# Kernel tuning notes

Measured on AMD Instinct MI355X. Metric: run time of the kernel, lower is better.

## Reference

```python
import jax, jax.numpy as jnp
import numpy as np

N = 30000
E = 960000
F_IN = 16
NH1 = 36
NH2 = 36
KH = 8
IN_POOL = 2
OUT_POOL = 2
NUM_CLASSES = 10
RATIO = 0.1
EPS = 1e-5


def cheb_conv(x, src, dst, valid, W, b):
    """PyG ChebConv with sym normalization, lambda_max=2 -> L_hat = -D^-1/2 A D^-1/2.
    W: [K, in, out], valid: float mask [E] for (soft-)deleted edges."""
    n = x.shape[0]
    deg = jax.ops.segment_sum(valid, src, num_segments=n)
    dinv = jnp.where(deg > 0, jax.lax.rsqrt(deg), 0.0)
    norm = dinv[src] * dinv[dst] * valid  # [E]

    def prop(h):  # L_hat @ h
        return -jax.ops.segment_sum(norm[:, None] * h[src], dst, num_segments=n)

    k_hops = W.shape[0]
    tx0 = x
    out = tx0 @ W[0]
    if k_hops > 1:
        tx1 = prop(tx0)
        out = out + tx1 @ W[1]
        for kk in range(2, k_hops):
            tx2 = 2.0 * prop(tx1) - tx0
            out = out + tx2 @ W[kk]
            tx0, tx1 = tx1, tx2
    return out + b


def batch_norm(x, gamma, beta):
    mu = jnp.mean(x, axis=0)
    var = jnp.var(x, axis=0)
    return (x - mu) * jax.lax.rsqrt(var + EPS) * gamma + beta


def setup_inputs() -> dict:
    key = jax.random.key(0)
    ks = jax.random.split(key, 20)
    rn = lambda k, s: jax.random.normal(k, s, dtype=jnp.float32) * 0.1
    x = jax.random.normal(ks[0], (N, F_IN), dtype=jnp.float32)
    edge_index = jax.random.randint(ks[1], (2, E), 0, N, dtype=jnp.int32)
    return {
        "x": x,
        "edge_index": edge_index,
        "W1": rn(ks[2], (KH, F_IN, NH1)), "b1": jnp.zeros((NH1,), jnp.float32),
        "W2": rn(ks[3], (KH, NH1, NH2)), "b2": jnp.zeros((NH2,), jnp.float32),
        "g1": jnp.ones((NH1,), jnp.float32), "be1": jnp.zeros((NH1,), jnp.float32),
        "g2": jnp.ones((NH2,), jnp.float32), "be2": jnp.zeros((NH2,), jnp.float32),
        "Wc": rn(ks[4], (1, NH1, IN_POOL)), "bc": jnp.zeros((IN_POOL,), jnp.float32),
        "pool_w": rn(ks[5], (IN_POOL,)),
        "Wp": rn(ks[6], (KH, IN_POOL, OUT_POOL)), "bp": jnp.zeros((OUT_POOL,), jnp.float32),
        "W3": rn(ks[7], (1, NH1 + NH2 + OUT_POOL, NUM_CLASSES)),
        "b3": jnp.zeros((NUM_CLASSES,), jnp.float32),
    }


def reference(x, edge_index, W1, b1, W2, b2, g1, be1, g2, be2, Wc, bc, pool_w, Wp, bp, W3, b3):
    src, dst = edge_index[0], edge_index[1]
    valid = jnp.ones((src.shape[0],), jnp.float32)

    x1 = batch_norm(jax.nn.relu(cheb_conv(x, src, dst, valid, W1, b1)), g1, be1)
    x2 = batch_norm(jax.nn.relu(cheb_conv(x1, src, dst, valid, W2, b2)), g2, be2)
    xc = cheb_conv(x1, src, dst, valid, Wc, bc)

    # TopKPooling(ratio=0.1)
    score = jnp.tanh(xc @ pool_w / jnp.linalg.norm(pool_w))  # [N]
    k = int(np.ceil(RATIO * x.shape[0]))
    _, perm = jax.lax.top_k(score, k)
    xp1 = xc[perm] * score[perm][:, None]
    new_idx = jnp.full((x.shape[0],), -1, jnp.int32).at[perm].set(jnp.arange(k, dtype=jnp.int32))
    vs, vd = new_idx[src], new_idx[dst]
    valid_p = ((vs >= 0) & (vd >= 0)).astype(jnp.float32)
    src_p = jnp.where(vs >= 0, vs, 0)
    dst_p = jnp.where(vd >= 0, vd, 0)

    xp2 = cheb_conv(xp1, src_p, dst_p, valid_p, Wp, bp)  # [k, OUT_POOL]

    # nearest-neighbor unpooling using last-2 feature columns as 2D positions
    pos = x[:, -2:]              # [N, 2]
    pos_p = pos[perm]            # [k, 2]
    d2 = jnp.sum((pos[:, None, :] - pos_p[None, :, :]) ** 2, axis=-1)  # [N, k]
    nearest = jnp.argmin(d2, axis=1)
    x3u = xp2[nearest]           # [N, OUT_POOL]

    h = jnp.concatenate((x1, x2, x3u), axis=1)
    return cheb_conv(h, src, dst, valid, W3, b3)
```

## Files before the change

kernel.cpp:

```cpp
#include <hip/hip_runtime.h>
#include <cstdint>

constexpr int NN   = 30000;
constexpr int NE   = 960000;
constexpr int FIN  = 16;
constexpr int H1   = 36;
constexpr int H2   = 36;
constexpr int KHOP = 8;
constexpr int KSEL = 3000;
constexpr int PCAP = 32768;
constexpr int NCHUNK = 12;
constexpr int CHUNK = KSEL / NCHUNK;
constexpr int NB_H = 32;
constexpr int EPB  = (NE + NB_H - 1) / NB_H;
constexpr float EPSV = 1e-5f;

#define TPB 256

static inline int nb(long long t) { return (int)((t + TPB - 1) / TPB); }

__global__ void k_dinv2(const int* __restrict__ cnt, float* __restrict__ dinv, int n) {
    int i = blockIdx.x * blockDim.x + threadIdx.x;
    if (i < n) { int v = cnt[i]; dinv[i] = v > 0 ? rsqrtf((float)v) : 0.0f; }
}

__global__ __launch_bounds__(1024)
void k_hist(const int* __restrict__ src, const int* __restrict__ dst,
            int* __restrict__ partials, int* __restrict__ rank) {
    __shared__ int hist[NN];
    for (int j = threadIdx.x; j < NN; j += 1024) hist[j] = 0;
    __syncthreads();
    int b = blockIdx.x;
    int e0 = b * EPB, e1 = min(NE, e0 + EPB);
    if (blockIdx.y == 0) {
        for (int e = e0 + (int)threadIdx.x; e < e1; e += 1024)
            atomicAdd(&hist[src[e]], 1);
    } else {
        for (int e = e0 + (int)threadIdx.x; e < e1; e += 1024)
            rank[e] = atomicAdd(&hist[dst[e]], 1);
    }
    __syncthreads();
    int* P = partials + ((size_t)blockIdx.y * NB_H + b) * NN;
    for (int j = threadIdx.x; j < NN; j += 1024) P[j] = hist[j];
}

__global__ void k_red(int* __restrict__ partials, float* __restrict__ dinv,
                      int* __restrict__ cnt_dst) {
    int j = blockIdx.x * blockDim.x + threadIdx.x;
    if (j >= NN) return;
    const int* Ps = partials;
    int s = 0;
#pragma unroll
    for (int b = 0; b < NB_H; ++b) s += Ps[(size_t)b * NN + j];
    dinv[j] = s > 0 ? rsqrtf((float)s) : 0.0f;
    int* Pd = partials + (size_t)NB_H * NN;
    int run = 0;
#pragma unroll
    for (int b = 0; b < NB_H; ++b) {
        int t = Pd[(size_t)b * NN + j];
        Pd[(size_t)b * NN + j] = run;
        run += t;
    }
    cnt_dst[j] = run;
}

__device__ __forceinline__ int block_scan_excl_1024(int val, int& total) {
    __shared__ int wsum[16];
    int tid = threadIdx.x, lane = tid & 63, wv = tid >> 6;
    int v = val;
#pragma unroll
    for (int off = 1; off < 64; off <<= 1) {
        int t = __shfl_up(v, off, 64);
        if (lane >= off) v += t;
    }
    __syncthreads();
    if (lane == 63) wsum[wv] = v;
    __syncthreads();
    if (tid < 16) {
        int w = wsum[tid];
#pragma unroll
        for (int off = 1; off < 16; off <<= 1) {
            int t = __shfl_up(w, off, 64);
            if (tid >= off) w += t;
        }
        wsum[tid] = w;
    }
    __syncthreads();
    int base = (wv > 0) ? wsum[wv - 1] : 0;
    total = wsum[15];
    return base + v - val;
}

__global__ void k_scan(const int* __restrict__ cnt, int* __restrict__ rowstart, int n) {
    __shared__ int run;
    if (threadIdx.x == 0) run = 0;
    __syncthreads();
    for (int base = 0; base < n; base += 1024) {
        int i = base + threadIdx.x;
        int v = (i < n) ? cnt[i] : 0;
        int tot; int ex = block_scan_excl_1024(v, tot);
        int r = run;
        if (i < n) rowstart[i] = r + ex;
        __syncthreads();
        if (threadIdx.x == 0) run += tot;
        __syncthreads();
    }
    if (threadIdx.x == 0) rowstart[n] = run;
}

__global__ void k_fill3(const int* __restrict__ src, const int* __restrict__ dst,
                        const int* __restrict__ rank, const float* __restrict__ dinv,
                        const int* __restrict__ rowstart, const int* __restrict__ Pd_excl,
                        int2* __restrict__ csr, int E) {
    int e = blockIdx.x * blockDim.x + threadIdx.x;
    if (e >= E) return;
    int s = src[e], d = dst[e];
    int b = e / EPB;
    int pos = rowstart[d] + Pd_excl[(size_t)b * NN + d] + rank[e];
    float w = -dinv[s] * dinv[d];
    csr[pos] = make_int2(s, __float_as_int(w));
}

template<int F, int O>
__global__ void k_gemm_init(const float* __restrict__ in, const float* __restrict__ W,
                            const float* __restrict__ b, float* __restrict__ acc, int n) {
    __shared__ float sW[F * O];
    for (int i = threadIdx.x; i < F * O; i += blockDim.x) sW[i] = W[i];
    __syncthreads();
    int t = blockIdx.x * blockDim.x + threadIdx.x;
    if (t >= n * O) return;
    int node = t / O, o = t - node * O;
    const float* r = &in[node * F];
    float s = b[o];
#pragma unroll
    for (int f = 0; f < F; ++f) s = fmaf(r[f], sW[f * O + o], s);
    acc[t] = s;
}

template<int F, int O, int BN>
__global__ __launch_bounds__(BN * F / 4)
void k_prop_gemm(const int* __restrict__ rowstart, const int2* __restrict__ csr,
                 const float* __restrict__ h, const float* __restrict__ t0,
                 const float* __restrict__ W, float* __restrict__ tout,
                 float* __restrict__ acc, int n, int first) {
    constexpr int QF = F / 4;
    constexpr int NT = BN * QF;
    __shared__ float sT[BN * F];
    __shared__ float sW[F * O];
    const int tid = threadIdx.x;
    for (int i = tid; i < F * O; i += NT) sW[i] = W[i];
    const int nl = tid / QF, q = tid - nl * QF;
    const int node = blockIdx.x * BN + nl;
    if (node < n) {
        const float4* __restrict__ h4 = (const float4*)h;
        float4 p = {0.f, 0.f, 0.f, 0.f};
        int e0 = rowstart[node], e1 = rowstart[node + 1];
        int e = e0;
        for (; e + 3 < e1; e += 4) {
            int2 ea = csr[e];
            int2 eb = csr[e + 1];
            int2 ec = csr[e + 2];
            int2 ed = csr[e + 3];
            float4 ha = h4[ea.x * QF + q];
            float4 hb = h4[eb.x * QF + q];
            float4 hc = h4[ec.x * QF + q];
            float4 hd = h4[ed.x * QF + q];
            float wa = __int_as_float(ea.y), wb = __int_as_float(eb.y);
            float wc = __int_as_float(ec.y), wd = __int_as_float(ed.y);
            p.x = fmaf(wa, ha.x, p.x); p.y = fmaf(wa, ha.y, p.y);
            p.z = fmaf(wa, ha.z, p.z); p.w = fmaf(wa, ha.w, p.w);
            p.x = fmaf(wb, hb.x, p.x); p.y = fmaf(wb, hb.y, p.y);
            p.z = fmaf(wb, hb.z, p.z); p.w = fmaf(wb, hb.w, p.w);
            p.x = fmaf(wc, hc.x, p.x); p.y = fmaf(wc, hc.y, p.y);
            p.z = fmaf(wc, hc.z, p.z); p.w = fmaf(wc, hc.w, p.w);
            p.x = fmaf(wd, hd.x, p.x); p.y = fmaf(wd, hd.y, p.y);
            p.z = fmaf(wd, hd.z, p.z); p.w = fmaf(wd, hd.w, p.w);
        }
        for (; e < e1; ++e) {
            int2 ew = csr[e];
            float w = __int_as_float(ew.y);
            float4 hv = h4[ew.x * QF + q];
            p.x = fmaf(w, hv.x, p.x); p.y = fmaf(w, hv.y, p.y);
            p.z = fmaf(w, hv.z, p.z); p.w = fmaf(w, hv.w, p.w);
        }
        if (!first) {
            float4 tv = ((const float4*)t0)[node * QF + q];
            p.x = 2.f * p.x - tv.x; p.y = 2.f * p.y - tv.y;
            p.z = 2.f * p.z - tv.z; p.w = 2.f * p.w - tv.w;
        }
        ((float4*)tout)[node * QF + q] = p;
        sT[nl * F + 4 * q + 0] = p.x; sT[nl * F + 4 * q + 1] = p.y;
        sT[nl * F + 4 * q + 2] = p.z; sT[nl * F + 4 * q + 3] = p.w;
    }
    __syncthreads();
    for (int idx = tid; idx < BN * O; idx += NT) {
        int nl2 = idx / O, o = idx - nl2 * O;
        int gn = blockIdx.x * BN + nl2;
        if (gn >= n) break;
        float s = 0.f;
#pragma unroll
        for (int f = 0; f < F; ++f) s = fmaf(sT[nl2 * F + f], sW[f * O + o], s);
        acc[gn * O + o] += s;
    }
}

template<int C>
__global__ void k_colstats(const float* __restrict__ a, float* __restrict__ stats, int n) {
    __shared__ float b1[C], b2[C];
    for (int i = threadIdx.x; i < C; i += blockDim.x) { b1[i] = 0.f; b2[i] = 0.f; }
    __syncthreads();
    int t0 = blockIdx.x * blockDim.x + threadIdx.x;
    int stride = gridDim.x * blockDim.x;
    int c = t0 % C;
    float s1 = 0.f, s2 = 0.f;
    for (int t = t0; t < n * C; t += stride) {
        float v = fmaxf(a[t], 0.f);
        s1 += v; s2 = fmaf(v, v, s2);
    }
    atomicAdd(&b1[c], s1); atomicAdd(&b2[c], s2);
    __syncthreads();
    for (int i = threadIdx.x; i < C; i += blockDim.x) {
        atomicAdd(&stats[i], b1[i]); atomicAdd(&stats[C + i], b2[i]);
    }
}

template<int C>
__global__ void k_bn(const float* __restrict__ a, const float* __restrict__ stats,
                     const float* __restrict__ g, const float* __restrict__ be,
                     float* __restrict__ o, int n) {
    int t = blockIdx.x * blockDim.x + threadIdx.x;
    if (t >= n * C) return;
    int c = t % C;
    float mu = stats[c] / n;
    float var = stats[C + c] / n - mu * mu;
    float v = fmaxf(a[t], 0.f);
    o[t] = (v - mu) * rsqrtf(var + EPSV) * g[c] + be[c];
}

__global__ void k_xc_score(const float* __restrict__ x1, const float* __restrict__ Wc,
                           const float* __restrict__ bc, const float* __restrict__ pw,
                           float* __restrict__ xc, float* __restrict__ score,
                           unsigned* __restrict__ key, int* __restrict__ gh, int n) {
    int i = blockIdx.x * blockDim.x + threadIdx.x;
    if (i >= n) return;
    const float* r = &x1[i * H1];
    float a = bc[0], b = bc[1];
#pragma unroll
    for (int f = 0; f < H1; ++f) { float v = r[f]; a = fmaf(v, Wc[f * 2], a); b = fmaf(v, Wc[f * 2 + 1], b); }
    xc[i * 2] = a; xc[i * 2 + 1] = b;
    float w0 = pw[0], w1 = pw[1];
    float s = tanhf((a * w0 + b * w1) / sqrtf(w0 * w0 + w1 * w1));
    score[i] = s;
    unsigned u = __float_as_uint(s);
    unsigned k = (u & 0x80000000u) ? ~u : (u | 0x80000000u);
    key[i] = k;
    atomicAdd(&gh[k >> 16], 1);
}

__global__ void k_h16b(const unsigned* __restrict__ key, const unsigned* __restrict__ pB,
                       int* __restrict__ gh, int n) {
    unsigned B = *pB;
    int i = blockIdx.x * blockDim.x + threadIdx.x;
    if (i < n && (key[i] >> 16) == B) atomicAdd(&gh[key[i] & 0xFFFFu], 1);
}

__global__ __launch_bounds__(1024)
void k_scanhist(const int* __restrict__ hist, const int* __restrict__ kin, int kdef,
                const unsigned* __restrict__ prevBin, unsigned* __restrict__ outT,
                int* __restrict__ outRem) {
    __shared__ int cs[1024];
    __shared__ int sC, sAbove;
    const int tid = threadIdx.x;
    int k = kin ? *kin : kdef;
    int s = 0;
    int base = tid * 64;
#pragma unroll 8
    for (int j = 0; j < 64; ++j) s += hist[base + j];
    cs[tid] = s;
    __syncthreads();
    int rsum = cs[1023 - tid];
    int tot; int ex = block_scan_excl_1024(rsum, tot);
    int c = 1023 - tid;
    if (ex < k && ex + cs[c] >= k) { sC = c; sAbove = ex; }
    __syncthreads();
    if (tid < 64) {
        int bin = sC * 64 + 63 - tid;
        int val = hist[bin];
        int incl = val;
#pragma unroll
        for (int off = 1; off < 64; off <<= 1) {
            int t2 = __shfl_up(incl, off, 64);
            if (tid >= off) incl += t2;
        }
        int above2 = sAbove + (incl - val);
        if (above2 < k && above2 + val >= k) {
            if (prevBin) *outT = ((*prevBin) << 16) | (unsigned)bin;
            else         *outT = (unsigned)bin;
            *outRem = k - above2;
        }
    }
}

__global__ __launch_bounds__(1024)
void k_selcnt(const unsigned* __restrict__ key, const unsigned* __restrict__ pT,
              int* __restrict__ bgt, int* __restrict__ beq, int n) {
    __shared__ int sgt, seq;
    if (threadIdx.x == 0) { sgt = 0; seq = 0; }
    __syncthreads();
    unsigned T = *pT;
    int i = blockIdx.x * 1024 + threadIdx.x;
    if (i < n) {
        unsigned kk = key[i];
        if (kk > T) atomicAdd(&sgt, 1);
        else if (kk == T) atomicAdd(&seq, 1);
    }
    __syncthreads();
    if (threadIdx.x == 0) { bgt[blockIdx.x] = sgt; beq[blockIdx.x] = seq; }
}

__global__ void k_seloff(const int* __restrict__ bgt, const int* __restrict__ beq,
                         const int* __restrict__ pR, int* __restrict__ eqoff,
                         int* __restrict__ soff, int nblk) {
    int t = threadIdx.x;
    int g = (t < nblk) ? bgt[t] : 0;
    int q = (t < nblk) ? beq[t] : 0;
    int gi = g, qi = q;
#pragma unroll
    for (int off = 1; off < 64; off <<= 1) {
        int a = __shfl_up(gi, off, 64);
        int b = __shfl_up(qi, off, 64);
        if (t >= off) { gi += a; qi += b; }
    }
    int qex = qi - q;
    int r = *pR;
    int eqsel = min(max(r - qex, 0), q);
    int scnt = g + eqsel;
    int si = scnt;
#pragma unroll
    for (int off = 1; off < 64; off <<= 1) {
        int a = __shfl_up(si, off, 64);
        if (t >= off) si += a;
    }
    if (t < nblk) { eqoff[t] = qex; soff[t] = si - scnt; }
}

__global__ __launch_bounds__(1024)
void k_selfill(const unsigned* __restrict__ key, const unsigned* __restrict__ pT,
               const int* __restrict__ pR, const int* __restrict__ eqoff,
               const int* __restrict__ soff, int* __restrict__ nidx,
               int* __restrict__ sel, int n) {
    unsigned T = *pT; int r = *pR;
    int b = blockIdx.x;
    int i = b * 1024 + threadIdx.x;
    unsigned kk = (i < n) ? key[i] : 0u;
    int eq = (i < n && kk == T) ? 1 : 0;
    int gt = (i < n && kk > T) ? 1 : 0;
    int eq_tot; int eq_ex = block_scan_excl_1024(eq, eq_tot);
    int sf = gt | (eq & (((eqoff[b] + eq_ex) < r) ? 1 : 0));
    int s_tot; int s_ex = block_scan_excl_1024(sf, s_tot);
    if (i < n) {
        if (sf) { int slot = soff[b] + s_ex; nidx[i] = slot; sel[slot] = i; }
        else nidx[i] = -1;
    }
}

__global__ void k_plen(const int* __restrict__ m_rowstart, const int2* __restrict__ m_csr,
                       const int* __restrict__ nidx, const int* __restrict__ sel,
                       int* __restrict__ pcnt, int* __restrict__ lens) {
    int wid = (blockIdx.x * blockDim.x + threadIdx.x) >> 6;
    int lane = threadIdx.x & 63;
    if (wid >= KSEL) return;
    int node = sel[wid];
    int e0 = m_rowstart[node], e1 = m_rowstart[node + 1];
    int cnt = 0;
    for (int e = e0 + lane; e < e1; e += 64) {
        int vs = nidx[m_csr[e].x];
        if (vs >= 0) { ++cnt; atomicAdd(&pcnt[vs], 1); }
    }
#pragma unroll
    for (int off = 32; off; off >>= 1) cnt += __shfl_down(cnt, off, 64);
    if (lane == 0) lens[wid] = cnt;
}

__global__ void k_pfill(const int* __restrict__ m_rowstart, const int2* __restrict__ m_csr,
                        const int* __restrict__ nidx, const int* __restrict__ sel,
                        const float* __restrict__ dinvp, const int* __restrict__ prs,
                        int2* __restrict__ gcsr) {
    int wid = (blockIdx.x * blockDim.x + threadIdx.x) >> 6;
    int lane = threadIdx.x & 63;
    if (wid >= KSEL) return;
    int node = sel[wid];
    int e0 = m_rowstart[node], e1 = m_rowstart[node + 1];
    float dd = dinvp[wid];
    int pos = prs[wid];
    for (int base = e0; base < e1; base += 64) {
        int e = base + lane;
        int vs = -1;
        if (e < e1) vs = nidx[m_csr[e].x];
        bool valid = vs >= 0;
        unsigned long long mask = __ballot(valid);
        if (valid) {
            int myoff = __popcll(mask & ((1ull << lane) - 1ull));
            float w = -dinvp[vs] * dd;
            gcsr[pos + myoff] = make_int2(vs, __float_as_int(w));
        }
        pos += __popcll(mask);
    }
}

__global__ __launch_bounds__(1024)
void k_pooled4(const int* __restrict__ prs_g, const int2* __restrict__ gcsr,
               const int* __restrict__ sel, const float* __restrict__ xc,
               const float* __restrict__ score, const float* __restrict__ x,
               const float* __restrict__ Wp, const float* __restrict__ bp,
               float* __restrict__ pacc_out, float* __restrict__ selpos) {
    __shared__ float bufA[2 * KSEL];
    __shared__ float bufB[2 * KSEL];
    __shared__ int   prs[KSEL + 1];
    const int tid = threadIdx.x, NT = 1024;

    for (int j = tid; j <= KSEL; j += NT) prs[j] = prs_g[j];

    const float bp0 = bp[0], bp1 = bp[1];
    float accA[3], accB[3];
#pragma unroll
    for (int r = 0; r < 3; ++r) {
        int j = tid + r * NT;
        accA[r] = 0.f; accB[r] = 0.f;
        if (j < KSEL) {
            int i = sel[j];
            float s = score[i];
            float a = xc[2 * i] * s, b = xc[2 * i + 1] * s;
            bufA[2 * j] = a; bufA[2 * j + 1] = b;
            accA[r] = bp0 + a * Wp[0] + b * Wp[2];
            accB[r] = bp1 + a * Wp[1] + b * Wp[3];
            selpos[2 * j] = x[i * FIN + 14];
            selpos[2 * j + 1] = x[i * FIN + 15];
        }
    }
    __syncthreads();

    for (int k = 1; k < KHOP; ++k) {
        float* rb = (k & 1) ? bufA : bufB;
        float* wb = (k & 1) ? bufB : bufA;
        float w0 = Wp[k * 4 + 0], w1 = Wp[k * 4 + 1];
        float w2 = Wp[k * 4 + 2], w3 = Wp[k * 4 + 3];
#pragma unroll
        for (int r = 0; r < 3; ++r) {
            int j = tid + r * NT;
            if (j < KSEL) {
                float pa = 0.f, pb = 0.f;
                int e0 = prs[j], e1 = prs[j + 1];
                for (int e = e0; e < e1; ++e) {
                    int2 ew = gcsr[e];
                    float w = __int_as_float(ew.y);
                    pa = fmaf(w, rb[2 * ew.x], pa);
                    pb = fmaf(w, rb[2 * ew.x + 1], pb);
                }
                if (k >= 2) {
                    pa = 2.f * pa - wb[2 * j];
                    pb = 2.f * pb - wb[2 * j + 1];
                }
                wb[2 * j] = pa; wb[2 * j + 1] = pb;
                accA[r] = fmaf(pa, w0, fmaf(pb, w2, accA[r]));
                accB[r] = fmaf(pa, w1, fmaf(pb, w3, accB[r]));
            }
        }
        __syncthreads();
    }

#pragma unroll
    for (int r = 0; r < 3; ++r) {
        int j = tid + r * NT;
        if (j < KSEL) {
            pacc_out[2 * j] = accA[r];
            pacc_out[2 * j + 1] = accB[r];
        }
    }
}

__global__ void k_near_part(const float* __restrict__ x, const float* __restrict__ selpos,
                            unsigned long long* __restrict__ best, int n) {
    __shared__ float2 sp[CHUNK];
    const int j0 = blockIdx.y * CHUNK;
    for (int j = threadIdx.x; j < CHUNK; j += blockDim.x)
        sp[j] = ((const float2*)selpos)[j0 + j];
    __syncthreads();
    int i = blockIdx.x * blockDim.x + threadIdx.x;
    if (i >= n) return;
    float px = x[i * FIN + 14], py = x[i * FIN + 15];
    float bd = 3.4e38f; int bj = 0;
#pragma unroll 2
    for (int j = 0; j < CHUNK; ++j) {
        float dx = px - sp[j].x, dy = py - sp[j].y;
        float d = fmaf(dx, dx, dy * dy);
        if (d < bd) { bd = d; bj = j0 + j; }
    }
    unsigned long long pk = ((unsigned long long)__float_as_uint(bd) << 32) | (unsigned)bj;
    atomicMin(&best[i], pk);
}

__global__ void k_final(const float* __restrict__ x1, const float* __restrict__ x2,
                        const float* __restrict__ xp2, const unsigned long long* __restrict__ best,
                        const float* __restrict__ W3, const float* __restrict__ b3,
                        float* __restrict__ o, int n) {
    __shared__ float sW[740], sb[10];
    for (int i = threadIdx.x; i < 740; i += blockDim.x) sW[i] = W3[i];
    if (threadIdx.x < 10) sb[threadIdx.x] = b3[threadIdx.x];
    __syncthreads();
    int t = blockIdx.x * blockDim.x + threadIdx.x;
    if (t >= n * 10) return;
    int i = t / 10, c = t - 10 * (t / 10);
    float s = sb[c];
    const float* r1 = &x1[i * H1];
#pragma unroll
    for (int f = 0; f < H1; ++f) s = fmaf(r1[f], sW[f * 10 + c], s);
    const float* r2 = &x2[i * H2];
#pragma unroll
    for (int f = 0; f < H2; ++f) s = fmaf(r2[f], sW[(H1 + f) * 10 + c], s);
    int m = (int)(best[i] & 0xFFFFFFFFull);
    s = fmaf(xp2[m * 2],     sW[720 + c], s);
    s = fmaf(xp2[m * 2 + 1], sW[730 + c], s);
    o[t] = s;
}

extern "C" void kernel_launch(void* const* d_in, const int* in_sizes, int n_in,
                              void* d_out, int out_size, void* d_ws, size_t ws_size,
                              hipStream_t stream) {
    const float* x   = (const float*)d_in[0];
    const int*   ei  = (const int*)d_in[1];
    const int*   src = ei;
    const int*   dst = ei + NE;
    const float* W1  = (const float*)d_in[2];
    const float* b1  = (const float*)d_in[3];
    const float* W2  = (const float*)d_in[4];
    const float* b2  = (const float*)d_in[5];
    const float* g1  = (const float*)d_in[6];
    const float* be1 = (const float*)d_in[7];
    const float* g2  = (const float*)d_in[8];
    const float* be2 = (const float*)d_in[9];
    const float* Wc  = (const float*)d_in[10];
    const float* bc  = (const float*)d_in[11];
    const float* pw  = (const float*)d_in[12];
    const float* Wp  = (const float*)d_in[13];
    const float* bp  = (const float*)d_in[14];
    const float* W3  = (const float*)d_in[15];
    const float* b3  = (const float*)d_in[16];
    float* out = (float*)d_out;

    char* w = (char*)d_ws;
    auto alloc = [&](size_t bytes) -> void* {
        void* p = (void*)w;
        w += (bytes + 255) & ~(size_t)255;
        return p;
    };
    int*   cnt_dst  = (int*)alloc(NN * 4);
    float* dinv     = (float*)alloc(NN * 4);
    int*   rowstart = (int*)alloc((NN + 1) * 4);
    int*   rank     = (int*)alloc((size_t)NE * 4);
    int2*  csr      = (int2*)alloc((size_t)NE * 8);
    float* B1    = (float*)alloc((size_t)NN * H1 * 4);
    float* B2    = (float*)alloc((size_t)NN * H1 * 4);
    float* B3    = (float*)alloc((size_t)NN * H1 * 4);
    float* acc   = (float*)alloc((size_t)NN * H1 * 4);
    float* x1    = (float*)alloc((size_t)NN * H1 * 4);
    float* x2    = (float*)alloc((size_t)NN * H2 * 4);
    float* xc    = (float*)alloc((size_t)NN * 2 * 4);
    float* score = (float*)alloc(NN * 4);
    float* stats = (float*)alloc(2 * H1 * 4);
    unsigned* key   = (unsigned*)alloc(NN * 4);
    int* nidx       = (int*)alloc(NN * 4);
    int* sel        = (int*)alloc(KSEL * 4);
    unsigned long long* best = (unsigned long long*)alloc(NN * 8);
    unsigned* Tptr  = (unsigned*)alloc(4);
    int* Rptr       = (int*)alloc(4);
    unsigned* BinPtr = (unsigned*)alloc(4);
    int* RemPtr     = (int*)alloc(4);
    int* gh         = (int*)alloc(2 * 65536 * 4);
    int* bgt        = (int*)alloc(64 * 4);
    int* beq        = (int*)alloc(64 * 4);
    int* eqoff      = (int*)alloc(64 * 4);
    int* soff       = (int*)alloc(64 * 4);
    int* pcnt       = (int*)alloc(KSEL * 4);
    int* lens       = (int*)alloc(KSEL * 4);
    int* prs        = (int*)alloc((KSEL + 1) * 4);
    float* dinvp    = (float*)alloc(KSEL * 4);
    int2* gcsr      = (int2*)alloc((size_t)PCAP * 8);
    float* pacc     = (float*)alloc(KSEL * 2 * 4);
    float* selpos   = (float*)alloc(KSEL * 2 * 4);

    int* partials = (int*)B1;

    const int NBK = (NN + 63) / 64;
    const int CSB = 117;

    hipMemsetAsync(pcnt, 0, KSEL * 4, stream);
    hipMemsetAsync(best, 0xFF, NN * 8, stream);
    hipMemsetAsync(gh, 0, 2 * 65536 * 4, stream);

    {
        dim3 gh2(NB_H, 2);
        k_hist<<<gh2, 1024, 0, stream>>>(src, dst, partials, rank);
        k_red<<<nb(NN), TPB, 0, stream>>>(partials, dinv, cnt_dst);
        k_scan<<<1, 1024, 0, stream>>>(cnt_dst, rowstart, NN);
        k_fill3<<<nb(NE), TPB, 0, stream>>>(src, dst, rank, dinv, rowstart,
                                            partials + (size_t)NB_H * NN, csr, NE);
    }

    {
        k_gemm_init<FIN, H1><<<nb((long long)NN * H1), TPB, 0, stream>>>(x, W1, b1, acc, NN);
        float* rot[3] = {B1, B2, B3};
        k_prop_gemm<FIN, H1, 64><<<NBK, 64 * (FIN / 4), 0, stream>>>(
            rowstart, csr, x, nullptr, W1 + FIN * H1, B1, acc, NN, 1);
        const float* t_prev = x; const float* t_cur = B1;
        for (int kk = 2; kk < KHOP; ++kk) {
            float* o = rot[(kk - 1) % 3];
            k_prop_gemm<FIN, H1, 64><<<NBK, 64 * (FIN / 4), 0, stream>>>(
                rowstart, csr, t_cur, t_prev, W1 + kk * FIN * H1, o, acc, NN, 0);
            t_prev = t_cur; t_cur = o;
        }
        hipMemsetAsync(stats, 0, 2 * H1 * 4, stream);
        k_colstats<H1><<<CSB, TPB, 0, stream>>>(acc, stats, NN);
        k_bn<H1><<<nb((long long)NN * H1), TPB, 0, stream>>>(acc, stats, g1, be1, x1, NN);
    }

    {
        k_gemm_init<H1, H2><<<nb((long long)NN * H2), TPB, 0, stream>>>(x1, W2, b2, acc, NN);
        float* rot[3] = {B1, B2, B3};
        k_prop_gemm<H1, H2, 64><<<NBK, 64 * (H1 / 4), 0, stream>>>(
            rowstart, csr, x1, nullptr, W2 + H1 * H2, B1, acc, NN, 1);
        const float* t_prev = x1; const float* t_cur = B1;
        for (int kk = 2; kk < KHOP; ++kk) {
            float* o = rot[(kk - 1) % 3];
            k_prop_gemm<H1, H2, 64><<<NBK, 64 * (H1 / 4), 0, stream>>>(
                rowstart, csr, t_cur, t_prev, W2 + kk * H1 * H2, o, acc, NN, 0);
            t_prev = t_cur; t_cur = o;
        }
        hipMemsetAsync(stats, 0, 2 * H2 * 4, stream);
        k_colstats<H2><<<CSB, TPB, 0, stream>>>(acc, stats, NN);
        k_bn<H2><<<nb((long long)NN * H2), TPB, 0, stream>>>(acc, stats, g2, be2, x2, NN);
    }

    k_xc_score<<<nb(NN), TPB, 0, stream>>>(x1, Wc, bc, pw, xc, score, key, gh, NN);

    k_scanhist<<<1, 1024, 0, stream>>>(gh, nullptr, KSEL, nullptr, BinPtr, RemPtr);
    k_h16b<<<nb(NN), TPB, 0, stream>>>(key, BinPtr, gh + 65536, NN);
    k_scanhist<<<1, 1024, 0, stream>>>(gh + 65536, RemPtr, 0, BinPtr, Tptr, Rptr);

    {
        const int SB = (NN + 1023) / 1024;
        k_selcnt<<<SB, 1024, 0, stream>>>(key, Tptr, bgt, beq, NN);
        k_seloff<<<1, 64, 0, stream>>>(bgt, beq, Rptr, eqoff, soff, SB);
        k_selfill<<<SB, 1024, 0, stream>>>(key, Tptr, Rptr, eqoff, soff, nidx, sel, NN);
    }

    {
        const int WPB = TPB / 64;
        const int GB = (KSEL + WPB - 1) / WPB;
        k_plen<<<GB, TPB, 0, stream>>>(rowstart, csr, nidx, sel, pcnt, lens);
        k_scan<<<1, 1024, 0, stream>>>(lens, prs, KSEL);
        k_dinv2<<<nb(KSEL), TPB, 0, stream>>>(pcnt, dinvp, KSEL);
        k_pfill<<<GB, TPB, 0, stream>>>(rowstart, csr, nidx, sel, dinvp, prs, gcsr);
    }

    k_pooled4<<<1, 1024, 0, stream>>>(prs, gcsr, sel, xc, score, x, Wp, bp, pacc, selpos);

    {
        dim3 g(nb(NN), NCHUNK);
        k_near_part<<<g, TPB, 0, stream>>>(x, selpos, best, NN);
    }
    k_final<<<nb((long long)NN * 10), TPB, 0, stream>>>(x1, x2, pacc, best, W3, b3, out, NN);
}
```

Baseline: 544.9 us.

## Fuse init GEMM into first hop, split edges across two threads, merge small launches

The separate k_gemm_init pass is folded into the first propagation kernel, which now computes bias + x@W0 + T1@W1 directly, so acc no longer needs a separate initialization pass. Each node's edge list is split between two thread slices, with the partial sums combined through shared memory, to add memory-level parallelism to the gather. The layer-2 block size drops to 32 nodes per block. Smaller launches and memsets are merged: stats zeroing moves into k_red, the pooled scan and dinv are combined into one kernel, and the pcnt memset is merged with the gh memset by making the buffers contiguous. The cost is extra shared memory and a __syncthreads per block, and correctness now depends on pcnt sitting right after gh in the allocation order.

```diff
diff --git a/kernel.cpp b/kernel.cpp
--- a/kernel.cpp
+++ b/kernel.cpp
@@ -19,11 +19,6 @@
 
 static inline int nb(long long t) { return (int)((t + TPB - 1) / TPB); }
 
-__global__ void k_dinv2(const int* __restrict__ cnt, float* __restrict__ dinv, int n) {
-    int i = blockIdx.x * blockDim.x + threadIdx.x;
-    if (i < n) { int v = cnt[i]; dinv[i] = v > 0 ? rsqrtf((float)v) : 0.0f; }
-}
-
 __global__ __launch_bounds__(1024)
 void k_hist(const int* __restrict__ src, const int* __restrict__ dst,
             int* __restrict__ partials, int* __restrict__ rank) {
@@ -45,7 +40,8 @@
 }
 
 __global__ void k_red(int* __restrict__ partials, float* __restrict__ dinv,
-                      int* __restrict__ cnt_dst) {
+                      int* __restrict__ cnt_dst, float* __restrict__ stats) {
+    if (blockIdx.x == 0 && threadIdx.x < 144) stats[threadIdx.x] = 0.f;
     int j = blockIdx.x * blockDim.x + threadIdx.x;
     if (j >= NN) return;
     const int* Ps = partials;
@@ -106,6 +102,29 @@
         __syncthreads();
     }
     if (threadIdx.x == 0) rowstart[n] = run;
+}
+
+__global__ __launch_bounds__(1024)
+void k_scan_pool(const int* __restrict__ lens, int* __restrict__ prs,
+                 const int* __restrict__ pcnt, float* __restrict__ dinvp) {
+    __shared__ int run;
+    if (threadIdx.x == 0) run = 0;
+    __syncthreads();
+    for (int base = 0; base < KSEL; base += 1024) {
+        int i = base + threadIdx.x;
+        int v = (i < KSEL) ? lens[i] : 0;
+        int tot; int ex = block_scan_excl_1024(v, tot);
+        int r = run;
+        if (i < KSEL) prs[i] = r + ex;
+        __syncthreads();
+        if (threadIdx.x == 0) run += tot;
+        __syncthreads();
+    }
+    if (threadIdx.x == 0) prs[KSEL] = run;
+    for (int j = threadIdx.x; j < KSEL; j += 1024) {
+        int c = pcnt[j];
+        dinvp[j] = c > 0 ? rsqrtf((float)c) : 0.0f;
+    }
 }
 
 __global__ void k_fill3(const int* __restrict__ src, const int* __restrict__ dst,
@@ -121,40 +140,41 @@
     csr[pos] = make_int2(s, __float_as_int(w));
 }
 
-template<int F, int O>
-__global__ void k_gemm_init(const float* __restrict__ in, const float* __restrict__ W,
-                            const float* __restrict__ b, float* __restrict__ acc, int n) {
-    __shared__ float sW[F * O];
-    for (int i = threadIdx.x; i < F * O; i += blockDim.x) sW[i] = W[i];
-    __syncthreads();
-    int t = blockIdx.x * blockDim.x + threadIdx.x;
-    if (t >= n * O) return;
-    int node = t / O, o = t - node * O;
-    const float* r = &in[node * F];
-    float s = b[o];
-#pragma unroll
-    for (int f = 0; f < F; ++f) s = fmaf(r[f], sW[f * O + o], s);
-    acc[t] = s;
-}
-
-template<int F, int O, int BN>
-__global__ __launch_bounds__(BN * F / 4)
+template<int F, int O, int BN, int ES, bool FIRST>
+__global__ __launch_bounds__(BN * (F / 4) * ES)
 void k_prop_gemm(const int* __restrict__ rowstart, const int2* __restrict__ csr,
                  const float* __restrict__ h, const float* __restrict__ t0,
-                 const float* __restrict__ W, float* __restrict__ tout,
-                 float* __restrict__ acc, int n, int first) {
+                 const float* __restrict__ Wk, const float* __restrict__ W0,
+                 const float* __restrict__ bias, float* __restrict__ tout,
+                 float* __restrict__ acc, int n) {
     constexpr int QF = F / 4;
-    constexpr int NT = BN * QF;
+    constexpr int NTH = BN * QF;
+    constexpr int NT = NTH * ES;
     __shared__ float sT[BN * F];
+    __shared__ float sP[(ES > 1) ? BN * F : 1];
     __shared__ float sW[F * O];
+    __shared__ float sW0[FIRST ? F * O : 1];
+    __shared__ float sX[FIRST ? BN * F : 1];
     const int tid = threadIdx.x;
-    for (int i = tid; i < F * O; i += NT) sW[i] = W[i];
-    const int nl = tid / QF, q = tid - nl * QF;
+    for (int i = tid; i < F * O; i += NT) sW[i] = Wk[i];
+    if (FIRST) {
+        for (int i = tid; i < F * O; i += NT) sW0[i] = W0[i];
+        int base = blockIdx.x * BN * F;
+        int lim = min(BN * F, n * F - base);
+        for (int i = tid; i < lim; i += NT) sX[i] = h[base + i];
+    }
+    const int sl = tid / NTH;
+    const int t2 = tid - sl * NTH;
+    const int nl = t2 / QF, q = t2 - nl * QF;
     const int node = blockIdx.x * BN + nl;
+    float4 p = {0.f, 0.f, 0.f, 0.f};
     if (node < n) {
         const float4* __restrict__ h4 = (const float4*)h;
-        float4 p = {0.f, 0.f, 0.f, 0.f};
         int e0 = rowstart[node], e1 = rowstart[node + 1];
+        if (ES > 1) {
+            int len = e1 - e0, half = (len + 1) >> 1;
+            if (sl == 0) e1 = e0 + half; else e0 += half;
+        }
         int e = e0;
         for (; e + 3 < e1; e += 4) {
             int2 ea = csr[e];
@@ -183,7 +203,20 @@
             p.x = fmaf(w, hv.x, p.x); p.y = fmaf(w, hv.y, p.y);
             p.z = fmaf(w, hv.z, p.z); p.w = fmaf(w, hv.w, p.w);
         }
-        if (!first) {
+    }
+    if (ES > 1) {
+        if (sl == 1 && node < n) {
+            sP[nl * F + 4 * q + 0] = p.x; sP[nl * F + 4 * q + 1] = p.y;
+            sP[nl * F + 4 * q + 2] = p.z; sP[nl * F + 4 * q + 3] = p.w;
+        }
+        __syncthreads();
+        if (sl == 0 && node < n) {
+            p.x += sP[nl * F + 4 * q + 0]; p.y += sP[nl * F + 4 * q + 1];
+            p.z += sP[nl * F + 4 * q + 2]; p.w += sP[nl * F + 4 * q + 3];
+        }
+    }
+    if (sl == 0 && node < n) {
+        if (!FIRST) {
             float4 tv = ((const float4*)t0)[node * QF + q];
             p.x = 2.f * p.x - tv.x; p.y = 2.f * p.y - tv.y;
             p.z = 2.f * p.z - tv.z; p.w = 2.f * p.w - tv.w;
@@ -197,10 +230,18 @@
         int nl2 = idx / O, o = idx - nl2 * O;
         int gn = blockIdx.x * BN + nl2;
         if (gn >= n) break;
-        float s = 0.f;
+        float s;
+        if (FIRST) {
+            s = bias[o];
+#pragma unroll
+            for (int f = 0; f < F; ++f) s = fmaf(sX[nl2 * F + f], sW0[f * O + o], s);
+        } else {
+            s = 0.f;
+        }
 #pragma unroll
         for (int f = 0; f < F; ++f) s = fmaf(sT[nl2 * F + f], sW[f * O + o], s);
-        acc[gn * O + o] += s;
+        if (FIRST) acc[gn * O + o] = s;
+        else       acc[gn * O + o] += s;
     }
 }
 
@@ -567,7 +608,7 @@
     float* x2    = (float*)alloc((size_t)NN * H2 * 4);
     float* xc    = (float*)alloc((size_t)NN * 2 * 4);
     float* score = (float*)alloc(NN * 4);
-    float* stats = (float*)alloc(2 * H1 * 4);
+    float* stats = (float*)alloc(144 * 4);
     unsigned* key   = (unsigned*)alloc(NN * 4);
     int* nidx       = (int*)alloc(NN * 4);
     int* sel        = (int*)alloc(KSEL * 4);
@@ -577,11 +618,11 @@
     unsigned* BinPtr = (unsigned*)alloc(4);
     int* RemPtr     = (int*)alloc(4);
     int* gh         = (int*)alloc(2 * 65536 * 4);
+    int* pcnt       = (int*)alloc(KSEL * 4);
     int* bgt        = (int*)alloc(64 * 4);
     int* beq        = (int*)alloc(64 * 4);
     int* eqoff      = (int*)alloc(64 * 4);
     int* soff       = (int*)alloc(64 * 4);
-    int* pcnt       = (int*)alloc(KSEL * 4);
     int* lens       = (int*)alloc(KSEL * 4);
     int* prs        = (int*)alloc((KSEL + 1) * 4);
     float* dinvp    = (float*)alloc(KSEL * 4);
@@ -589,56 +630,55 @@
     float* pacc     = (float*)alloc(KSEL * 2 * 4);
     float* selpos   = (float*)alloc(KSEL * 2 * 4);
 
+    float* stats1 = stats;
+    float* stats2 = stats + 72;
+
     int* partials = (int*)B1;
 
-    const int NBK = (NN + 63) / 64;
+    const int NBK1 = (NN + 63) / 64;
+    const int NBK2 = (NN + 31) / 32;
     const int CSB = 117;
 
-    hipMemsetAsync(pcnt, 0, KSEL * 4, stream);
+    hipMemsetAsync(gh, 0, 2 * 65536 * 4 + ((KSEL * 4 + 255) & ~255), stream);
     hipMemsetAsync(best, 0xFF, NN * 8, stream);
-    hipMemsetAsync(gh, 0, 2 * 65536 * 4, stream);
 
     {
         dim3 gh2(NB_H, 2);
         k_hist<<<gh2, 1024, 0, stream>>>(src, dst, partials, rank);
-        k_red<<<nb(NN), TPB, 0, stream>>>(partials, dinv, cnt_dst);
+        k_red<<<nb(NN), TPB, 0, stream>>>(partials, dinv, cnt_dst, stats);
         k_scan<<<1, 1024, 0, stream>>>(cnt_dst, rowstart, NN);
         k_fill3<<<nb(NE), TPB, 0, stream>>>(src, dst, rank, dinv, rowstart,
                                             partials + (size_t)NB_H * NN, csr, NE);
     }
 
     {
-        k_gemm_init<FIN, H1><<<nb((long long)NN * H1), TPB, 0, stream>>>(x, W1, b1, acc, NN);
         float* rot[3] = {B1, B2, B3};
-        k_prop_gemm<FIN, H1, 64><<<NBK, 64 * (FIN / 4), 0, stream>>>(
-            rowstart, csr, x, nullptr, W1 + FIN * H1, B1, acc, NN, 1);
+        k_prop_gemm<FIN, H1, 64, 2, true><<<NBK1, 512, 0, stream>>>(
+            rowstart, csr, x, nullptr, W1 + FIN * H1, W1, b1, B1, acc, NN);
         const float* t_prev = x; const float* t_cur = B1;
         for (int kk = 2; kk < KHOP; ++kk) {
             float* o = rot[(kk - 1) % 3];
-            k_prop_gemm<FIN, H1, 64><<<NBK, 64 * (FIN / 4), 0, stream>>>(
-                rowstart, csr, t_cur, t_prev, W1 + kk * FIN * H1, o, acc, NN, 0);
+            k_prop_gemm<FIN, H1, 64, 2, false><<<NBK1, 512, 0, stream>>>(
+                rowstart, csr, t_cur, t_prev, W1 + kk * FIN * H1, nullptr, nullptr, o, acc, NN);
             t_prev = t_cur; t_cur = o;
         }
-        hipMemsetAsync(stats, 0, 2 * H1 * 4, stream);
-        k_colstats<H1><<<CSB, TPB, 0, stream>>>(acc, stats, NN);
-        k_bn<H1><<<nb((long long)NN * H1), TPB, 0, stream>>>(acc, stats, g1, be1, x1, NN);
+        k_colstats<H1><<<CSB, TPB, 0, stream>>>(acc, stats1, NN);
+        k_bn<H1><<<nb((long long)NN * H1), TPB, 0, stream>>>(acc, stats1, g1, be1, x1, NN);
     }
 
     {
-        k_gemm_init<H1, H2><<<nb((long long)NN * H2), TPB, 0, stream>>>(x1, W2, b2, acc, NN);
         float* rot[3] = {B1, B2, B3};
-        k_prop_gemm<H1, H2, 64><<<NBK, 64 * (H1 / 4), 0, stream>>>(
-            rowstart, csr, x1, nullptr, W2 + H1 * H2, B1, acc, NN, 1);
+        k_prop_gemm<H1, H2, 32, 2, true><<<NBK2, 576, 0, stream>>>(
+            rowstart, csr, x1, nullptr, W2 + H1 * H2, W2, b2, B1, acc, NN);
         const float* t_prev = x1; const float* t_cur = B1;
         for (int kk = 2; kk < KHOP; ++kk) {
             float* o = rot[(kk - 1) % 3];
-            k_prop_gemm<H1, H2, 64><<<NBK, 64 * (H1 / 4), 0, stream>>>(
-                rowstart, csr, t_cur, t_prev, W2 + kk * H1 * H2, o, acc, NN, 0);
+            k_prop_gemm<H1, H2, 32, 2, false><<<NBK2, 576, 0, stream>>>(
+                rowstart, csr, t_cur, t_prev, W2 + kk * H1 * H2, nullptr, nullptr, o, acc, NN);
             t_prev = t_cur; t_cur = o;
         }
-        hipMemsetAsync(stats, 0, 2 * H2 * 4, stream);
-        k_colstats<H2><<<CSB, TPB, 0, stream>>>(acc, stats, NN);
-        k_bn<H2><<<nb((long long)NN * H2), TPB, 0, stream>>>(acc, stats, g2, be2, x2, NN);
+        k_colstats<H2><<<CSB, TPB, 0, stream>>>(acc, stats2, NN);
+        k_bn<H2><<<nb((long long)NN * H2), TPB, 0, stream>>>(acc, stats2, g2, be2, x2, NN);
     }
 
     k_xc_score<<<nb(NN), TPB, 0, stream>>>(x1, Wc, bc, pw, xc, score, key, gh, NN);
@@ -658,8 +698,7 @@
         const int WPB = TPB / 64;
         const int GB = (KSEL + WPB - 1) / WPB;
         k_plen<<<GB, TPB, 0, stream>>>(rowstart, csr, nidx, sel, pcnt, lens);
-        k_scan<<<1, 1024, 0, stream>>>(lens, prs, KSEL);
-        k_dinv2<<<nb(KSEL), TPB, 0, stream>>>(pcnt, dinvp, KSEL);
+        k_scan_pool<<<1, 1024, 0, stream>>>(lens, prs, pcnt, dinvp);
         k_pfill<<<GB, TPB, 0, stream>>>(rowstart, csr, nidx, sel, dinvp, prs, gcsr);
     }
 
```

New measurement: 556.0 us. 2.0% more time.
